# Optimization experiments

Measured on AMD Instinct MI355X. Metric: run time of the kernel, lower is better.

The kernel has to match this reference:

```python
import jax, jax.numpy as jnp
import numpy as np

N, E, VD, HD, ES = 10000, 80000, 32, 64, 68
NET_IN = VD * VD + 2 * HD + ES   # 1220: f2s(1024) + s[e0](64) + s[e1](64) + edge_s(68)
SELF_IN = VD * VD + 2 * HD       # 1152: temp_f2s(1024) + s(64) + s_c(64)
OUT_D = VD * VD + HD             # 1088: vector channel mixer + scalar update


def _lecun(k, fin, fout):
    return jax.random.normal(k, (fin, fout), jnp.float32) / jnp.sqrt(jnp.float32(fin))


def setup_inputs() -> dict:
    ks = jax.random.split(jax.random.key(0), 16)
    return {
        "f": jax.random.normal(ks[0], (N, 3, VD), jnp.float32),
        "s": jax.random.normal(ks[1], (N, HD), jnp.float32),
        "edge_f": jax.random.normal(ks[2], (E, 3, 1), jnp.float32),
        "edge_s": jax.random.normal(ks[3], (E, ES), jnp.float32),
        "W_emb1": _lecun(ks[4], 2 * VD + 1, VD),
        "net_W1": _lecun(ks[5], NET_IN, HD), "net_b1": jnp.zeros((HD,), jnp.float32),
        "net_W2": _lecun(ks[6], HD, HD), "net_b2": jnp.zeros((HD,), jnp.float32),
        "net_W3": _lecun(ks[7], HD, OUT_D), "net_b3": jnp.zeros((OUT_D,), jnp.float32),
        "W_emb2": _lecun(ks[8], 2 * VD, VD),
        "self_W1": _lecun(ks[9], SELF_IN, HD), "self_b1": jnp.zeros((HD,), jnp.float32),
        "self_W2": _lecun(ks[10], HD, HD), "self_b2": jnp.zeros((HD,), jnp.float32),
        "self_W3": _lecun(ks[11], HD, OUT_D), "self_b3": jnp.zeros((OUT_D,), jnp.float32),
        "edge_index": jax.random.randint(ks[12], (2, E), 0, N),
    }


def _mlp(x, W1, b1, W2, b2, W3, b3):
    h = jax.nn.relu(x @ W1 + b1)
    h = jax.nn.relu(h @ W2 + b2)
    return h @ W3 + b3


def _segment_mean(x, ids, n):
    tot = jax.ops.segment_sum(x, ids, num_segments=n)
    cnt = jax.ops.segment_sum(jnp.ones(ids.shape, x.dtype), ids, num_segments=n)
    return tot / jnp.maximum(cnt, 1.0).reshape((n,) + (1,) * (x.ndim - 1))


def _forward(f, s, edge_f, edge_s,
             W_emb1, net_W1, net_b1, net_W2, net_b2, net_W3, net_b3,
             W_emb2, self_W1, self_b1, self_W2, self_b2, self_W3, self_b3,
             edge_index):
    n = f.shape[0]
    e0, e1 = edge_index[0], edge_index[1]
    # --- edge message: gather -> embed -> gram einsum -> MLP ---
    _f = jnp.concatenate((f[e0], f[e1], edge_f), axis=-1)          # [E,3,2VD+1]
    _s = jnp.concatenate((s[e0], s[e1], edge_s), axis=-1)          # [E,2HD+ES]
    _f = _f @ W_emb1                                               # [E,3,VD]
    f2s = jnp.einsum('eij,eik->ejk', _f, _f).reshape(-1, VD * VD)  # _f^T @ _f, [E,VD*VD]
    Fn = jnp.linalg.norm(f2s, axis=-1, keepdims=True) + 1.0
    c = _mlp(jnp.concatenate((f2s, _s), axis=-1),
             net_W1, net_b1, net_W2, net_b2, net_W3, net_b3) / Fn  # [E,OUT_D]
    f_c = jnp.einsum('eij,ejk->eik', _f, c[:, :VD * VD].reshape(-1, VD, VD))  # [E,3,VD]
    f_c = _segment_mean(f_c, e0, n)                                # [N,3,VD]
    s_c = _segment_mean(c[:, VD * VD:], e0, n)                     # [N,HD]
    # --- node self-update ---
    tf = jnp.concatenate((f, f_c), axis=-1) @ W_emb2               # [N,3,VD]
    tf2s = jnp.einsum('nij,nik->njk', tf, tf).reshape(n, VD * VD)
    Fn2 = jnp.linalg.norm(tf2s, axis=-1, keepdims=True) + 1.0
    c2 = _mlp(jnp.concatenate((tf2s, s, s_c), axis=-1),
              self_W1, self_b1, self_W2, self_b2, self_W3, self_b3) / Fn2
    f_out = jnp.einsum('nij,njk->nik', tf, c2[:, :VD * VD].reshape(-1, VD, VD)) + f
    s_out = c2[:, VD * VD:] + s
    return f_out, s_out


def reference(f, s, edge_f, edge_s,
              W_emb1, net_W1, net_b1, net_W2, net_b2, net_W3, net_b3,
              W_emb2, self_W1, self_b1, self_W2, self_b2, self_W3, self_b3,
              edge_index):
    return _forward(f, s, edge_f, edge_s,
                    W_emb1, net_W1, net_b1, net_W2, net_b2, net_W3, net_b3,
                    W_emb2, self_W1, self_b1, self_W2, self_b2, self_W3, self_b3,
                    edge_index)
```

## Files before the change

### kernel.cpp

```cpp
#include <hip/hip_runtime.h>
#include <math.h>

#define NN 10000
#define NE 80000
#define SFH 102
#define SFB 98
#define SSB 66
#define STX 72
#define NTRI 528
#define SAE 104
#define SAN 72

typedef __attribute__((ext_vector_type(8))) __bf16 bf16x8;
typedef __attribute__((ext_vector_type(8))) short short8v;
typedef __attribute__((ext_vector_type(4))) float f32x4;
typedef __attribute__((ext_vector_type(4))) unsigned uint4v;

__device__ __forceinline__ ushort f2bf(float x) {
  union { float f; unsigned u; } v; v.f = x;
  unsigned r = v.u + 0x7FFFu + ((v.u >> 16) & 1u);
  return (ushort)(r >> 16);
}
__device__ __forceinline__ float bfu(ushort u) {
  union { unsigned x; float f; } v; v.x = (unsigned)u << 16;
  return v.f;
}
__device__ __forceinline__ void tri_ab(int k, int& a, int& b) {
  int aa = 0, rem = k;
  while (rem >= 32 - aa) { rem -= 32 - aa; ++aa; }
  a = aa; b = aa + rem;
}

__global__ __launch_bounds__(1024)
void sgnn_scan(const int* __restrict__ deg, int* __restrict__ cursor,
               int* __restrict__ start) {
  __shared__ int sm[1024];
  const int t = threadIdx.x;
  const int i0 = t * 10;
  int v[10], pre = 0;
  #pragma unroll
  for (int q = 0; q < 10; ++q) {
    const int i = i0 + q;
    v[q] = (i < NN) ? deg[i] : 0;
    pre += v[q];
  }
  sm[t] = pre;
  __syncthreads();
  int run = pre;
  #pragma unroll
  for (int d = 1; d < 1024; d <<= 1) {
    const int add = (t >= d) ? sm[t - d] : 0;
    __syncthreads();
    run += add;
    sm[t] = run;
    __syncthreads();
  }
  int excl = run - pre;
  #pragma unroll
  for (int q = 0; q < 10; ++q) {
    const int i = i0 + q;
    if (i < NN) { cursor[i] = excl; start[i] = excl; }
    excl += v[q];
  }
}

__global__ __launch_bounds__(256)
void sgnn_scatter(const int* __restrict__ eidx, int* __restrict__ cursor,
                  int* __restrict__ sorted) {
  const int e = blockIdx.x * 256 + threadIdx.x;
  if (e < NE) {
    const int p = atomicAdd(cursor + eidx[e], 1);
    sorted[p] = e;
  }
}

__global__ __launch_bounds__(256)
void sgnn_wconv(const float* __restrict__ nW1, const float* __restrict__ nW2,
                const float* __restrict__ nW3, const float* __restrict__ sW1,
                const float* __restrict__ sW2, const float* __restrict__ sW3,
                const float* __restrict__ Wemb1, const float* __restrict__ Wemb2,
                const int* __restrict__ eidx, int* __restrict__ deg,
                ushort* __restrict__ wout, ushort* __restrict__ tab) {
  const int gid = blockIdx.x * 256 + threadIdx.x;
  if (gid < NE) atomicAdd(deg + eidx[gid], 1);
  if (gid >= 61 * 4096) {
    const int k = gid - 61 * 4096;
    if (k < NTRI) {
      int a, b; tri_ab(k, a, b);
      tab[k] = (ushort)(a | (b << 8) | ((a != b) ? 0x8000 : 0));
    }
    return;
  }
  const int tile = gid >> 12, idx = gid & 4095;
  const int c = idx >> 6, k = idx & 63;
  float v = 0.f;
  if (tile < 12) {
    const int T = tile;
    if (T < 8 || (T == 8 && k < 16)) {
      const int ktri = T * 64 + k;
      if (ktri < NTRI) {
        int a, b; tri_ab(ktri, a, b);
        v = nW1[(a * 32 + b) * 64 + c];
        if (a != b) v += nW1[(b * 32 + a) * 64 + c];
      }
    } else if (T == 8) { if (k < 20) v = nW1[(1216 + (k - 16)) * 64 + c]; }
    else if (T == 9)   v = nW1[(1024 + k) * 64 + c];
    else if (T == 10)  v = nW1[(1088 + k) * 64 + c];
    else               v = nW1[(1152 + k) * 64 + c];
  } else if (tile == 12) v = nW2[k * 64 + c];
  else if (tile < 30)    v = nW3[k * 1088 + (tile - 13) * 64 + c];
  else if (tile < 41) {
    const int T = tile - 30;
    if (T < 8 || (T == 8 && k < 16)) {
      const int ktri = T * 64 + k;
      if (ktri < NTRI) {
        int a, b; tri_ab(ktri, a, b);
        v = sW1[(a * 32 + b) * 64 + c];
        if (a != b) v += sW1[(b * 32 + a) * 64 + c];
      }
    } else if (T == 9) v = sW1[(1024 + k) * 64 + c];
    else if (T == 10)  v = sW1[(1088 + k) * 64 + c];
  } else if (tile == 41) v = sW2[k * 64 + c];
  else if (tile < 59)    v = sW3[k * 1088 + (tile - 42) * 64 + c];
  else if (tile == 59) {
    const int col = idx / 96, kk = idx % 96;
    v = (col < 32 && kk < 65) ? Wemb1[kk * 32 + col] : 0.f;
  } else {
    const int col = idx >> 6;
    v = (col < 32) ? Wemb2[k * 32 + col] : 0.f;
  }
  wout[gid] = f2bf(v);
}

#define STAGE_W(srcbase) do { const ushort* _s = (srcbase);                      \
  _Pragma("unroll") for (int rr = 0; rr < 2; ++rr) {                             \
    const int idx_ = t + 256 * rr; const int c_ = idx_ >> 3, ko_ = idx_ & 7;     \
    *(short8v*)&Wl[c_ * STX + ko_ * 8] = *(const short8v*)&_s[c_ * 64 + ko_ * 8];\
  } } while (0)

#define WPRE_LOAD(srcbase) do { const ushort* _s = (srcbase);                    \
  wpre0 = *(const short8v*)&_s[(t >> 3) * 64 + (t & 7) * 8];                     \
  wpre1 = *(const short8v*)&_s[(32 + (t >> 3)) * 64 + (t & 7) * 8]; } while (0)

#define WPRE_STORE() do {                                                        \
  *(short8v*)&Wl[(t >> 3) * STX + (t & 7) * 8] = wpre0;                          \
  *(short8v*)&Wl[(32 + (t >> 3)) * STX + (t & 7) * 8] = wpre1; } while (0)

#define MFMA_K64_RA() do {                                                       \
  acc[0] = __builtin_amdgcn_mfma_f32_16x16x32_bf16(af0.v8,                       \
      *(const bf16x8*)&Wl[(     ll) * STX + lh * 8], acc[0], 0, 0, 0);           \
  acc[1] = __builtin_amdgcn_mfma_f32_16x16x32_bf16(af0.v8,                       \
      *(const bf16x8*)&Wl[(16 + ll) * STX + lh * 8], acc[1], 0, 0, 0);           \
  acc[2] = __builtin_amdgcn_mfma_f32_16x16x32_bf16(af0.v8,                       \
      *(const bf16x8*)&Wl[(32 + ll) * STX + lh * 8], acc[2], 0, 0, 0);           \
  acc[3] = __builtin_amdgcn_mfma_f32_16x16x32_bf16(af0.v8,                       \
      *(const bf16x8*)&Wl[(48 + ll) * STX + lh * 8], acc[3], 0, 0, 0);           \
  acc[0] = __builtin_amdgcn_mfma_f32_16x16x32_bf16(af1.v8,                       \
      *(const bf16x8*)&Wl[(     ll) * STX + 32 + lh * 8], acc[0], 0, 0, 0);      \
  acc[1] = __builtin_amdgcn_mfma_f32_16x16x32_bf16(af1.v8,                       \
      *(const bf16x8*)&Wl[(16 + ll) * STX + 32 + lh * 8], acc[1], 0, 0, 0);      \
  acc[2] = __builtin_amdgcn_mfma_f32_16x16x32_bf16(af1.v8,                       \
      *(const bf16x8*)&Wl[(32 + ll) * STX + 32 + lh * 8], acc[2], 0, 0, 0);      \
  acc[3] = __builtin_amdgcn_mfma_f32_16x16x32_bf16(af1.v8,                       \
      *(const bf16x8*)&Wl[(48 + ll) * STX + 32 + lh * 8], acc[3], 0, 0, 0);      \
} while (0)

#define MFMA_K64() do {                                                          \
  _Pragma("unroll") for (int kb = 0; kb < 2; ++kb) {                             \
    const bf16x8 af_ = *(const bf16x8*)&Xl[(w * 16 + ll) * STX + kb * 32 + lh * 8]; \
    acc[0] = __builtin_amdgcn_mfma_f32_16x16x32_bf16(af_,                        \
        *(const bf16x8*)&Wl[(     ll) * STX + kb * 32 + lh * 8], acc[0], 0, 0, 0); \
    acc[1] = __builtin_amdgcn_mfma_f32_16x16x32_bf16(af_,                        \
        *(const bf16x8*)&Wl[(16 + ll) * STX + kb * 32 + lh * 8], acc[1], 0, 0, 0); \
    acc[2] = __builtin_amdgcn_mfma_f32_16x16x32_bf16(af_,                        \
        *(const bf16x8*)&Wl[(32 + ll) * STX + kb * 32 + lh * 8], acc[2], 0, 0, 0); \
    acc[3] = __builtin_amdgcn_mfma_f32_16x16x32_bf16(af_,                        \
        *(const bf16x8*)&Wl[(48 + ll) * STX + kb * 32 + lh * 8], acc[3], 0, 0, 0); \
  } } while (0)

#define ZERO_ACC() do { _Pragma("unroll") for (int q = 0; q < 4; ++q)            \
    acc[q] = (f32x4){0.f, 0.f, 0.f, 0.f}; } while (0)

#define PACK_STORE16(dstp) do {                                                  \
  unsigned pk[8];                                                                \
  _Pragma("unroll") for (int q = 0; q < 8; ++q)                                  \
    pk[q] = (unsigned)f2bf(xv[2 * q]) | ((unsigned)f2bf(xv[2 * q + 1]) << 16);   \
  *(uint4v*)(dstp)       = (uint4v){pk[0], pk[1], pk[2], pk[3]};                 \
  *(uint4v*)((dstp) + 8) = (uint4v){pk[4], pk[5], pk[6], pk[7]};                 \
} while (0)

#define PACK_AF() do {                                                           \
  _Pragma("unroll") for (int q2 = 0; q2 < 4; ++q2) {                             \
    af0.u[q2] = (unsigned)f2bf(xv[2 * q2]) | ((unsigned)f2bf(xv[2 * q2 + 1]) << 16); \
    af1.u[q2] = (unsigned)f2bf(xv[8 + 2 * q2]) | ((unsigned)f2bf(xv[8 + 2 * q2 + 1]) << 16); \
  } } while (0)

#define TRI8(kt, off) do {                                                       \
  int prev_a = -1; float fa0 = 0.f, fa1 = 0.f, fa2 = 0.f;                        \
  _Pragma("unroll") for (int q = 0; q < 8; ++q) {                                \
    const int tb = tabL[(kt) + q];                                               \
    const int a_ = tb & 31, b_ = (tb >> 8) & 31;                                 \
    if (a_ != prev_a) { fa0 = bfu(frA[a_]); fa1 = bfu(frA[32 + a_]);             \
                        fa2 = bfu(frA[64 + a_]); prev_a = a_; }                  \
    const float v = fmaf(fa0, bfu(frA[b_]),                                      \
        fmaf(fa1, bfu(frA[32 + b_]), fa2 * bfu(frA[64 + b_])));                  \
    const float wsel = (tb & 0x8000) ? 2.f : 1.f;                                \
    sumsq = fmaf(v * wsel, v, sumsq);                                            \
    xv[(off) + q] = v;                                                           \
  } } while (0)

#define XV8_LOAD(p, off) do { const float* _p = (p);                             \
  const float4 va = *(const float4*)(_p);                                        \
  const float4 vb = *(const float4*)(_p + 4);                                    \
  xv[(off)+0]=va.x; xv[(off)+1]=va.y; xv[(off)+2]=va.z; xv[(off)+3]=va.w;        \
  xv[(off)+4]=vb.x; xv[(off)+5]=vb.y; xv[(off)+6]=vb.z; xv[(off)+7]=vb.w;        \
} while (0)

#define XV_LOAD16(p) do { const float* _p = (p);                                 \
  _Pragma("unroll") for (int q = 0; q < 4; ++q) {                                \
    const float4 v4 = *(const float4*)(_p + 4 * q);                              \
    xv[4 * q + 0] = v4.x; xv[4 * q + 1] = v4.y;                                  \
    xv[4 * q + 2] = v4.z; xv[4 * q + 3] = v4.w; } } while (0)

#define CONSUME_NT() do {                                                        \
  _Pragma("unroll") for (int r = 0; r < 4; ++r) {                                \
    const int row_ = w * 16 + lh * 4 + r;                                        \
    const unsigned u0 = *(const unsigned*)&smFh[row_ * SFH +      nt * 2];       \
    const unsigned u1 = *(const unsigned*)&smFh[row_ * SFH + 32 + nt * 2];       \
    const unsigned u2 = *(const unsigned*)&smFh[row_ * SFH + 64 + nt * 2];       \
    union { unsigned x; float f; } l0, h0, l1, h1, l2, h2;                       \
    l0.x = u0 << 16; h0.x = u0 & 0xffff0000u;                                    \
    l1.x = u1 << 16; h1.x = u1 & 0xffff0000u;                                    \
    l2.x = u2 << 16; h2.x = u2 & 0xffff0000u;                                    \
    _Pragma("unroll") for (int nc = 0; nc < 4; ++nc) {                           \
      const float cv = (acc[nc][r] + b3v[nc]) * ifnr[r];                         \
      const int p = nc & 1;                                                      \
      const float f0 = (nc < 2) ? l0.f : h0.f;                                   \
      const float f1 = (nc < 2) ? l1.f : h1.f;                                   \
      const float f2 = (nc < 2) ? l2.f : h2.f;                                   \
      fch[(r * 3 + 0) * 2 + p] = fmaf(f0, cv, fch[(r * 3 + 0) * 2 + p]);         \
      fch[(r * 3 + 1) * 2 + p] = fmaf(f1, cv, fch[(r * 3 + 1) * 2 + p]);         \
      fch[(r * 3 + 2) * 2 + p] = fmaf(f2, cv, fch[(r * 3 + 2) * 2 + p]);         \
    }                                                                            \
  } } while (0)

#define STAGE_FS() do {                                                          \
  _Pragma("unroll") for (int r = 0; r < 4; ++r) {                                \
    const int row_ = w * 16 + lh * 4 + r;                                        \
    _Pragma("unroll") for (int i = 0; i < 3; ++i) {                              \
      F[row_ * SFB + i * 32 + ll]      = f2bf(fch[(r * 3 + i) * 2 + 0]);         \
      F[row_ * SFB + i * 32 + ll + 16] = f2bf(fch[(r * 3 + i) * 2 + 1]);         \
    }                                                                            \
    _Pragma("unroll") for (int nc = 0; nc < 4; ++nc)                             \
      S[row_ * SSB + nc * 16 + ll] = f2bf(cs[nc * 4 + r]);                       \
  } } while (0)

#define LDS_BYTES 34656

__global__ __launch_bounds__(256, 3)
void sgnn_edge(const float* __restrict__ f, const float* __restrict__ s,
               const float* __restrict__ edge_f, const float* __restrict__ edge_s,
               const float* __restrict__ b1, const float* __restrict__ b2,
               const float* __restrict__ b3,
               const ushort* __restrict__ wbf, const ushort* __restrict__ tab_g,
               const int* __restrict__ eidx, const int* __restrict__ sorted,
               const int* __restrict__ start_g, const int* __restrict__ deg_g,
               float* __restrict__ fc_sum, float* __restrict__ sc_sum) {
  __shared__ __align__(16) char sbuf[LDS_BYTES];
  ushort* smFh = (ushort*)sbuf;
  ushort* F    = (ushort*)sbuf;
  ushort* Xl   = (ushort*)(sbuf + 13056);
  ushort* S    = (ushort*)(sbuf + 13056);
  ushort* Aemb = (ushort*)(sbuf + 13056);
  ushort* Wl   = (ushort*)(sbuf + 22272);
  int*    snode = (int*)(sbuf + 31488);
  int*    srow0 = snode + 8;
  int*    srow1 = snode + 16;
  int*    sst   = snode + 24;
  int*    sdg   = snode + 32;
  ushort* tabL = (ushort*)(sbuf + 33088);
  float*  iFn  = (float*)(sbuf + 33088);
  int*    es_s = (int*)(sbuf + 34144);
  ushort* e0s  = (ushort*)(sbuf + 34400);
  ushort* e1s  = (ushort*)(sbuf + 34528);

  const int t = threadIdx.x, j = t & 63, w = t >> 6, eb = w * 16;
  const int lh = j >> 4, ll = j & 15;
  const int bid = blockIdx.x;
  const ushort* wembT = wbf + 59 * 4096;
  short8v wpre0, wpre1;

  if (t < 64) {
    const int e = sorted[bid * 64 + t];
    es_s[t] = e;
    e0s[t] = (ushort)eidx[e];
    e1s[t] = (ushort)eidx[NE + e];
  }
  for (int idx = t; idx < NTRI; idx += 256) tabL[idx] = tab_g[idx];
  __syncthreads();

  int str = 0, dgr = 0;
  if (j < 16) {
    const int n_ = e0s[eb + j];
    str = start_g[n_];
    dgr = deg_g[n_];
  }
  WPRE_LOAD(wbf + 0);

  #pragma unroll 1
  for (int h = 0; h < 2; ++h) {
    const int hb = h * 32;
    #pragma unroll 1
    for (int cc = t; cc < 576; cc += 256) {
      const int row = cc / 6, seg = cc - row * 6;
      const int lel = (row * 43) >> 7, il = row - lel * 3;
      const int k0 = seg * 16;
      float xv[16];
      if (seg < 4) {
        const int nd = (seg < 2) ? (int)e0s[hb + lel] : (int)e1s[hb + lel];
        XV_LOAD16(f + nd * 96 + il * 32 + (seg & 1) * 16);
      } else if (seg == 4) {
        xv[0] = edge_f[es_s[hb + lel] * 3 + il];
        #pragma unroll
        for (int m = 1; m < 16; ++m) xv[m] = 0.f;
      } else {
        #pragma unroll
        for (int m = 0; m < 16; ++m) xv[m] = 0.f;
      }
      PACK_STORE16(&Aemb[row * SAE + k0]);
    }
    __syncthreads();
    #pragma unroll 1
    for (int job = w * 3; job < w * 3 + 3; ++job) {
      const int mt = job >> 1, nt = job & 1;
      f32x4 ac = (f32x4){0.f, 0.f, 0.f, 0.f};
      #pragma unroll
      for (int kb = 0; kb < 3; ++kb) {
        const bf16x8 av = *(const bf16x8*)&Aemb[(mt * 16 + ll) * SAE + kb * 32 + lh * 8];
        const bf16x8 bv = *(const bf16x8*)&wembT[(nt * 16 + ll) * 96 + kb * 32 + lh * 8];
        ac = __builtin_amdgcn_mfma_f32_16x16x32_bf16(av, bv, ac, 0, 0, 0);
      }
      #pragma unroll
      for (int r = 0; r < 4; ++r) {
        const int rr = mt * 16 + lh * 4 + r;
        const int lel = (rr * 43) >> 7, il = rr - lel * 3;
        smFh[(hb + lel) * SFH + il * 32 + nt * 16 + ll] = f2bf(ac[r]);
      }
    }
    __syncthreads();
  }

  f32x4 acc[4];
  ZERO_ACC();
  float sumsq = 0.f;
  const int rowA = w * 16 + ll;
  const ushort* frA = smFh + rowA * SFH;

  #pragma unroll 1
  for (int T = 0; T < 12; ++T) {
    float xv[16];
    union { unsigned u[4]; bf16x8 v8; } af0, af1;
    if (T < 8) {
      TRI8(T * 64 + lh * 8, 0);
      TRI8(T * 64 + 32 + lh * 8, 8);
    } else if (T == 8) {
      #pragma unroll
      for (int kb2 = 0; kb2 < 2; ++kb2)
        #pragma unroll
        for (int q = 0; q < 8; ++q) {
          const int k = kb2 * 32 + lh * 8 + q;
          float v = 0.f;
          if (k < 16) {
            const int tb = tabL[512 + k];
            const int a_ = tb & 31, b_ = (tb >> 8) & 31;
            v = fmaf(bfu(frA[a_]), bfu(frA[b_]),
                fmaf(bfu(frA[32 + a_]), bfu(frA[32 + b_]),
                     bfu(frA[64 + a_]) * bfu(frA[64 + b_])));
            const float wsel = (tb & 0x8000) ? 2.f : 1.f;
            sumsq = fmaf(v * wsel, v, sumsq);
          } else if (k < 20) {
            v = edge_s[es_s[rowA] * 68 + 64 + (k - 16)];
          }
          xv[kb2 * 8 + q] = v;
        }
    } else {
      const float* p = (T == 9)  ? (s + e0s[rowA] * 64)
                     : (T == 10) ? (s + e1s[rowA] * 64)
                                 : (edge_s + es_s[rowA] * 68);
      XV8_LOAD(p + lh * 8, 0);
      XV8_LOAD(p + 32 + lh * 8, 8);
    }
    PACK_AF();
    __syncthreads();
    WPRE_STORE();
    __syncthreads();
    WPRE_LOAD(wbf + (T + 1) * 4096);
    MFMA_K64_RA();
  }

  {
    float ss = sumsq;
    ss += __shfl_xor(ss, 16);
    ss += __shfl_xor(ss, 32);
    __syncthreads();
    if (j < 16) iFn[eb + j] = 1.f / (sqrtf(ss) + 1.f);
  }
  #pragma unroll
  for (int nc = 0; nc < 4; ++nc) {
    const float bv = b1[nc * 16 + ll];
    #pragma unroll
    for (int r = 0; r < 4; ++r)
      Xl[(w * 16 + lh * 4 + r) * STX + nc * 16 + ll] = f2bf(fmaxf(acc[nc][r] + bv, 0.f));
  }
  WPRE_STORE();
  ZERO_ACC();
  __syncthreads();
  WPRE_LOAD(wbf + 13 * 4096);

  MFMA_K64();
  #pragma unroll
  for (int nc = 0; nc < 4; ++nc) {
    const float bv = b2[nc * 16 + ll];
    #pragma unroll
    for (int r = 0; r < 4; ++r)
      Xl[(w * 16 + lh * 4 + r) * STX + nc * 16 + ll] = f2bf(fmaxf(acc[nc][r] + bv, 0.f));
  }

  float fch[24];
  #pragma unroll
  for (int q = 0; q < 24; ++q) fch[q] = 0.f;
  float cs[16];
  float ifnr[4];

  #pragma unroll 1
  for (int nt = 0; nt < 17; ++nt) {
    __syncthreads();
    WPRE_STORE();
    float b3v[4];
    #pragma unroll
    for (int nc = 0; nc < 4; ++nc) b3v[nc] = b3[nt * 64 + nc * 16 + ll];
    __syncthreads();
    if (nt < 16) WPRE_LOAD(wbf + (14 + nt) * 4096);
    if (nt == 0) {
      #pragma unroll
      for (int r = 0; r < 4; ++r) ifnr[r] = iFn[w * 16 + lh * 4 + r];
    }
    ZERO_ACC();
    MFMA_K64();
    if (nt < 16) {
      CONSUME_NT();
    } else {
      #pragma unroll
      for (int nc = 0; nc < 4; ++nc)
        #pragma unroll
        for (int r = 0; r < 4; ++r)
          cs[nc * 4 + r] = (acc[nc][r] + b3v[nc]) * ifnr[r];
    }
  }

  __syncthreads();
  STAGE_FS();
  if (t < 8) snode[t] = -1;
  __syncthreads();

  {
    float r0 = 0.f, r1 = 0.f, rs = 0.f;
    int runlen = 0;
    const int gwb = bid * 64 + eb;
    #pragma unroll 1
    for (int m = 0; m < 16; ++m) {
      const int row = eb + m;
      r0 += bfu(F[row * SFB + j]);
      if (j < 32) r1 += bfu(F[row * SFB + 64 + j]);
      rs += bfu(S[row * SSB + j]);
      ++runlen;
      const int n = e0s[row];
      if (m == 15 || e0s[row + 1] != n) {
        const int st = __shfl(str, m);
        const int dg = __shfl(dgr, m);
        const int g1v = gwb + m, g0v = g1v - runlen + 1;
        if (g0v == st && runlen == dg) {
          fc_sum[n * 96 + j] = r0;
          if (j < 32) fc_sum[n * 96 + 64 + j] = r1;
          sc_sum[n * 64 + j] = rs;
        } else {
          const int slot = (g0v == gwb) ? 2 * w : 2 * w + 1;
          if (j == 0) {
            snode[slot] = n; srow0[slot] = row - runlen + 1; srow1[slot] = row;
            sst[slot] = st; sdg[slot] = dg;
          }
        }
        r0 = r1 = rs = 0.f; runlen = 0;
      }
    }
  }
  __syncthreads();

  if (t < 160) {
    const int ch = t;
    int prevn = -1;
    #pragma unroll 1
    for (int ss = 0; ss < 8; ++ss) {
      const int n = snode[ss];
      if (n < 0) continue;
      if (n != prevn) {
        float v = 0.f;
        #pragma unroll 1
        for (int k2 = ss; k2 < 8; ++k2) {
          if (snode[k2] == n) {
            #pragma unroll 1
            for (int row = srow0[k2]; row <= srow1[k2]; ++row)
              v += (ch < 96) ? bfu(F[row * SFB + ch]) : bfu(S[row * SSB + (ch - 96)]);
          } else if (k2 > ss && snode[k2] >= 0) break;
        }
        const bool cib = (sst[ss] >= bid * 64) && (sst[ss] + sdg[ss] <= bid * 64 + 64);
        float* dst = (ch < 96) ? (fc_sum + n * 96 + ch) : (sc_sum + n * 64 + (ch - 96));
        if (cib) *dst = v; else atomicAdd(dst, v);
      }
      prevn = n;
    }
  }
}

__global__ __launch_bounds__(256, 3)
void sgnn_node(const float* __restrict__ f, const float* __restrict__ s,
               const float* __restrict__ b1, const float* __restrict__ b2,
               const float* __restrict__ b3,
               const ushort* __restrict__ wbf, const ushort* __restrict__ tab_g,
               const float* __restrict__ fcm, const float* __restrict__ scm,
               const int* __restrict__ deg_g,
               float* __restrict__ of, float* __restrict__ os) {
  __shared__ __align__(16) char sbuf[LDS_BYTES];
  ushort* smFh = (ushort*)sbuf;
  ushort* F    = (ushort*)sbuf;
  ushort* Xl   = (ushort*)(sbuf + 13056);
  ushort* S    = (ushort*)(sbuf + 13056);
  ushort* Aemb = (ushort*)(sbuf + 13056);
  ushort* Wl   = (ushort*)(sbuf + 22272);
  float*  icntL = (float*)(sbuf + 31488);
  ushort* tabL = (ushort*)(sbuf + 33088);
  float*  iFn  = (float*)(sbuf + 33088);

  const int t = threadIdx.x, j = t & 63, w = t >> 6, eb = w * 16;
  const int lh = j >> 4, ll = j & 15;
  const int nbase = blockIdx.x * 64;
  const ushort* wembTn = wbf + 60 * 4096;
  short8v wpre0, wpre1;

  for (int idx = t; idx < NTRI; idx += 256) tabL[idx] = tab_g[idx];
  if (t < 64)
    icntL[t] = 1.f / fmaxf((float)deg_g[min(nbase + t, NN - 1)], 1.f);
  WPRE_LOAD(wbf + 30 * 4096);
  __syncthreads();

  #pragma unroll 1
  for (int h = 0; h < 2; ++h) {
    const int hb = h * 32;
    #pragma unroll 1
    for (int cc = t; cc < 384; cc += 256) {
      const int row = cc >> 2, seg = cc & 3;
      const int lel = (row * 43) >> 7, il = row - lel * 3;
      const int nc = min(nbase + hb + lel, NN - 1);
      const int k0 = seg * 16;
      float xv[16];
      if (seg < 2) {
        XV_LOAD16(f + nc * 96 + il * 32 + seg * 16);
      } else {
        XV_LOAD16(fcm + nc * 96 + il * 32 + (seg - 2) * 16);
        const float ic = icntL[hb + lel];
        #pragma unroll
        for (int m = 0; m < 16; ++m) xv[m] *= ic;
      }
      PACK_STORE16(&Aemb[row * SAN + k0]);
    }
    __syncthreads();
    #pragma unroll 1
    for (int job = w * 3; job < w * 3 + 3; ++job) {
      const int mt = job >> 1, nt = job & 1;
      f32x4 ac = (f32x4){0.f, 0.f, 0.f, 0.f};
      #pragma unroll
      for (int kb = 0; kb < 2; ++kb) {
        const bf16x8 av = *(const bf16x8*)&Aemb[(mt * 16 + ll) * SAN + kb * 32 + lh * 8];
        const bf16x8 bv = *(const bf16x8*)&wembTn[(nt * 16 + ll) * 64 + kb * 32 + lh * 8];
        ac = __builtin_amdgcn_mfma_f32_16x16x32_bf16(av, bv, ac, 0, 0, 0);
      }
      #pragma unroll
      for (int r = 0; r < 4; ++r) {
        const int rr = mt * 16 + lh * 4 + r;
        const int lel = (rr * 43) >> 7, il = rr - lel * 3;
        smFh[(hb + lel) * SFH + il * 32 + nt * 16 + ll] = f2bf(ac[r]);
      }
    }
    __syncthreads();
  }

  f32x4 acc[4];
  ZERO_ACC();
  float sumsq = 0.f;
  const int rowA = w * 16 + ll;
  const ushort* frA = smFh + rowA * SFH;
  const int ncA = min(nbase + rowA, NN - 1);

  #pragma unroll 1
  for (int T = 0; T < 11; ++T) {
    float xv[16];
    union { unsigned u[4]; bf16x8 v8; } af0, af1;
    if (T < 8) {
      TRI8(T * 64 + lh * 8, 0);
      TRI8(T * 64 + 32 + lh * 8, 8);
    } else if (T == 8) {
      #pragma unroll
      for (int kb2 = 0; kb2 < 2; ++kb2)
        #pragma unroll
        for (int q = 0; q < 8; ++q) {
          const int k = kb2 * 32 + lh * 8 + q;
          float v = 0.f;
          if (k < 16) {
            const int tb = tabL[512 + k];
            const int a_ = tb & 31, b_ = (tb >> 8) & 31;
            v = fmaf(bfu(frA[a_]), bfu(frA[b_]),
                fmaf(bfu(frA[32 + a_]), bfu(frA[32 + b_]),
                     bfu(frA[64 + a_]) * bfu(frA[64 + b_])));
            const float wsel = (tb & 0x8000) ? 2.f : 1.f;
            sumsq = fmaf(v * wsel, v, sumsq);
          }
          xv[kb2 * 8 + q] = v;
        }
    } else if (T == 9) {
      XV8_LOAD(s + ncA * 64 + lh * 8, 0);
      XV8_LOAD(s + ncA * 64 + 32 + lh * 8, 8);
    } else {
      const float ic = icntL[rowA];
      XV8_LOAD(scm + ncA * 64 + lh * 8, 0);
      XV8_LOAD(scm + ncA * 64 + 32 + lh * 8, 8);
      #pragma unroll
      for (int m = 0; m < 16; ++m) xv[m] *= ic;
    }
    PACK_AF();
    __syncthreads();
    WPRE_STORE();
    __syncthreads();
    WPRE_LOAD(wbf + (31 + T) * 4096);
    MFMA_K64_RA();
  }

  {
    float ss = sumsq;
    ss += __shfl_xor(ss, 16);
    ss += __shfl_xor(ss, 32);
    __syncthreads();
    if (j < 16) iFn[eb + j] = 1.f / (sqrtf(ss) + 1.f);
  }
  #pragma unroll
  for (int nc = 0; nc < 4; ++nc) {
    const float bv = b1[nc * 16 + ll];
    #pragma unroll
    for (int r = 0; r < 4; ++r)
      Xl[(w * 16 + lh * 4 + r) * STX + nc * 16 + ll] = f2bf(fmaxf(acc[nc][r] + bv, 0.f));
  }
  WPRE_STORE();
  ZERO_ACC();
  __syncthreads();
  WPRE_LOAD(wbf + 42 * 4096);

  MFMA_K64();
  #pragma unroll
  for (int nc = 0; nc < 4; ++nc) {
    const float bv = b2[nc * 16 + ll];
    #pragma unroll
    for (int r = 0; r < 4; ++r)
      Xl[(w * 16 + lh * 4 + r) * STX + nc * 16 + ll] = f2bf(fmaxf(acc[nc][r] + bv, 0.f));
  }

  float fch[24];
  #pragma unroll
  for (int q = 0; q < 24; ++q) fch[q] = 0.f;
  float cs[16];
  float ifnr[4];

  #pragma unroll 1
  for (int nt = 0; nt < 17; ++nt) {
    __syncthreads();
    WPRE_STORE();
    float b3v[4];
    #pragma unroll
    for (int nc = 0; nc < 4; ++nc) b3v[nc] = b3[nt * 64 + nc * 16 + ll];
    __syncthreads();
    if (nt < 16) WPRE_LOAD(wbf + (43 + nt) * 4096);
    if (nt == 0) {
      #pragma unroll
      for (int r = 0; r < 4; ++r) ifnr[r] = iFn[w * 16 + lh * 4 + r];
    }
    ZERO_ACC();
    MFMA_K64();
    if (nt < 16) {
      CONSUME_NT();
    } else {
      #pragma unroll
      for (int nc = 0; nc < 4; ++nc)
        #pragma unroll
        for (int r = 0; r < 4; ++r)
          cs[nc * 4 + r] = (acc[nc][r] + b3v[nc]) * ifnr[r];
    }
  }

  __syncthreads();
  STAGE_FS();
  __syncthreads();

  #pragma unroll 1
  for (int m = 0; m < 16; ++m) {
    const int row = eb + m;
    const int n_m = nbase + row;
    if (n_m < NN) {
      of[n_m * 96 + j] = bfu(F[row * SFB + j]) + f[n_m * 96 + j];
      if (j < 32)
        of[n_m * 96 + 64 + j] = bfu(F[row * SFB + 64 + j]) + f[n_m * 96 + 64 + j];
      os[n_m * 64 + j] = bfu(S[row * SSB + j]) + s[n_m * 64 + j];
    }
  }
}

extern "C" void kernel_launch(void* const* d_in, const int* in_sizes, int n_in,
                              void* d_out, int out_size, void* d_ws, size_t ws_size,
                              hipStream_t stream) {
  const float* f      = (const float*)d_in[0];
  const float* s      = (const float*)d_in[1];
  const float* edge_f = (const float*)d_in[2];
  const float* edge_s = (const float*)d_in[3];
  const float* Wemb1  = (const float*)d_in[4];
  const float* nW1 = (const float*)d_in[5];
  const float* nb1 = (const float*)d_in[6];
  const float* nW2 = (const float*)d_in[7];
  const float* nb2 = (const float*)d_in[8];
  const float* nW3 = (const float*)d_in[9];
  const float* nb3 = (const float*)d_in[10];
  const float* Wemb2 = (const float*)d_in[11];
  const float* sW1 = (const float*)d_in[12];
  const float* sb1 = (const float*)d_in[13];
  const float* sW2 = (const float*)d_in[14];
  const float* sb2 = (const float*)d_in[15];
  const float* sW3 = (const float*)d_in[16];
  const float* sb3 = (const float*)d_in[17];
  const int* eidx  = (const int*)d_in[18];

  float* of = (float*)d_out;
  float* os = of + (size_t)NN * 96;

  int* deg    = (int*)d_ws;
  int* cursor = deg + NN;
  int* start  = cursor + NN;
  int* sorted = start + NN;
  ushort* wbf = (ushort*)(sorted + NE);
  ushort* tab = wbf + 61 * 4096;

  hipMemsetAsync(deg, 0, (size_t)NN * 4, stream);
  hipMemsetAsync(d_out, 0, (size_t)NN * 160 * 4, stream);

  hipLaunchKernelGGL(sgnn_wconv, dim3((61 * 4096 + NTRI + 255) / 256), dim3(256),
                     0, stream, nW1, nW2, nW3, sW1, sW2, sW3, Wemb1, Wemb2,
                     eidx, deg, wbf, tab);
  hipLaunchKernelGGL(sgnn_scan, dim3(1), dim3(1024), 0, stream, deg, cursor, start);
  hipLaunchKernelGGL(sgnn_scatter, dim3((NE + 255) / 256), dim3(256), 0, stream,
                     eidx, cursor, sorted);
  hipLaunchKernelGGL(sgnn_edge, dim3(NE / 64), dim3(256), 0, stream,
                     f, s, edge_f, edge_s, nb1, nb2, nb3,
                     wbf, tab, eidx, sorted, start, deg,
                     of , os );
  hipLaunchKernelGGL(sgnn_node, dim3((NN + 63) / 64), dim3(256), 0, stream,
                     f, s, sb1, sb2, sb3,
                     wbf, tab, of , os , deg, of, os);
}
```

Baseline: 198.0 us.

## Double-buffer LDS weight tiles to halve barriers in MLP loops

```diff
diff --git a/kernel.cpp b/kernel.cpp
--- a/kernel.cpp
+++ b/kernel.cpp
@@ -132,50 +132,44 @@
   wout[gid] = f2bf(v);
 }
 
-#define STAGE_W(srcbase) do { const ushort* _s = (srcbase);                      \
-  _Pragma("unroll") for (int rr = 0; rr < 2; ++rr) {                             \
-    const int idx_ = t + 256 * rr; const int c_ = idx_ >> 3, ko_ = idx_ & 7;     \
-    *(short8v*)&Wl[c_ * STX + ko_ * 8] = *(const short8v*)&_s[c_ * 64 + ko_ * 8];\
-  } } while (0)
-
 #define WPRE_LOAD(srcbase) do { const ushort* _s = (srcbase);                    \
   wpre0 = *(const short8v*)&_s[(t >> 3) * 64 + (t & 7) * 8];                     \
   wpre1 = *(const short8v*)&_s[(32 + (t >> 3)) * 64 + (t & 7) * 8]; } while (0)
 
-#define WPRE_STORE() do {                                                        \
-  *(short8v*)&Wl[(t >> 3) * STX + (t & 7) * 8] = wpre0;                          \
-  *(short8v*)&Wl[(32 + (t >> 3)) * STX + (t & 7) * 8] = wpre1; } while (0)
-
-#define MFMA_K64_RA() do {                                                       \
+#define WPRE_STORE_TO(Wd) do { ushort* _d = (Wd);                                \
+  *(short8v*)&_d[(t >> 3) * STX + (t & 7) * 8] = wpre0;                          \
+  *(short8v*)&_d[(32 + (t >> 3)) * STX + (t & 7) * 8] = wpre1; } while (0)
+
+#define MFMA_K64_RA_B(Wb) do { const ushort* _wl = (Wb);                         \
   acc[0] = __builtin_amdgcn_mfma_f32_16x16x32_bf16(af0.v8,                       \
-      *(const bf16x8*)&Wl[(     ll) * STX + lh * 8], acc[0], 0, 0, 0);           \
+      *(const bf16x8*)&_wl[(     ll) * STX + lh * 8], acc[0], 0, 0, 0);          \
   acc[1] = __builtin_amdgcn_mfma_f32_16x16x32_bf16(af0.v8,                       \
-      *(const bf16x8*)&Wl[(16 + ll) * STX + lh * 8], acc[1], 0, 0, 0);           \
+      *(const bf16x8*)&_wl[(16 + ll) * STX + lh * 8], acc[1], 0, 0, 0);          \
   acc[2] = __builtin_amdgcn_mfma_f32_16x16x32_bf16(af0.v8,                       \
-      *(const bf16x8*)&Wl[(32 + ll) * STX + lh * 8], acc[2], 0, 0, 0);           \
+      *(const bf16x8*)&_wl[(32 + ll) * STX + lh * 8], acc[2], 0, 0, 0);          \
   acc[3] = __builtin_amdgcn_mfma_f32_16x16x32_bf16(af0.v8,                       \
-      *(const bf16x8*)&Wl[(48 + ll) * STX + lh * 8], acc[3], 0, 0, 0);           \
+      *(const bf16x8*)&_wl[(48 + ll) * STX + lh * 8], acc[3], 0, 0, 0);          \
   acc[0] = __builtin_amdgcn_mfma_f32_16x16x32_bf16(af1.v8,                       \
-      *(const bf16x8*)&Wl[(     ll) * STX + 32 + lh * 8], acc[0], 0, 0, 0);      \
+      *(const bf16x8*)&_wl[(     ll) * STX + 32 + lh * 8], acc[0], 0, 0, 0);     \
   acc[1] = __builtin_amdgcn_mfma_f32_16x16x32_bf16(af1.v8,                       \
-      *(const bf16x8*)&Wl[(16 + ll) * STX + 32 + lh * 8], acc[1], 0, 0, 0);      \
+      *(const bf16x8*)&_wl[(16 + ll) * STX + 32 + lh * 8], acc[1], 0, 0, 0);     \
   acc[2] = __builtin_amdgcn_mfma_f32_16x16x32_bf16(af1.v8,                       \
-      *(const bf16x8*)&Wl[(32 + ll) * STX + 32 + lh * 8], acc[2], 0, 0, 0);      \
+      *(const bf16x8*)&_wl[(32 + ll) * STX + 32 + lh * 8], acc[2], 0, 0, 0);     \
   acc[3] = __builtin_amdgcn_mfma_f32_16x16x32_bf16(af1.v8,                       \
-      *(const bf16x8*)&Wl[(48 + ll) * STX + 32 + lh * 8], acc[3], 0, 0, 0);      \
+      *(const bf16x8*)&_wl[(48 + ll) * STX + 32 + lh * 8], acc[3], 0, 0, 0);     \
 } while (0)
 
-#define MFMA_K64() do {                                                          \
+#define MFMA_K64_B(Xb, Wb) do { const ushort* _x = (Xb); const ushort* _wl = (Wb);\
   _Pragma("unroll") for (int kb = 0; kb < 2; ++kb) {                             \
-    const bf16x8 af_ = *(const bf16x8*)&Xl[(w * 16 + ll) * STX + kb * 32 + lh * 8]; \
+    const bf16x8 af_ = *(const bf16x8*)&_x[(w * 16 + ll) * STX + kb * 32 + lh * 8]; \
     acc[0] = __builtin_amdgcn_mfma_f32_16x16x32_bf16(af_,                        \
-        *(const bf16x8*)&Wl[(     ll) * STX + kb * 32 + lh * 8], acc[0], 0, 0, 0); \
+        *(const bf16x8*)&_wl[(     ll) * STX + kb * 32 + lh * 8], acc[0], 0, 0, 0); \
     acc[1] = __builtin_amdgcn_mfma_f32_16x16x32_bf16(af_,                        \
-        *(const bf16x8*)&Wl[(16 + ll) * STX + kb * 32 + lh * 8], acc[1], 0, 0, 0); \
+        *(const bf16x8*)&_wl[(16 + ll) * STX + kb * 32 + lh * 8], acc[1], 0, 0, 0); \
     acc[2] = __builtin_amdgcn_mfma_f32_16x16x32_bf16(af_,                        \
-        *(const bf16x8*)&Wl[(32 + ll) * STX + kb * 32 + lh * 8], acc[2], 0, 0, 0); \
+        *(const bf16x8*)&_wl[(32 + ll) * STX + kb * 32 + lh * 8], acc[2], 0, 0, 0); \
     acc[3] = __builtin_amdgcn_mfma_f32_16x16x32_bf16(af_,                        \
-        *(const bf16x8*)&Wl[(48 + ll) * STX + kb * 32 + lh * 8], acc[3], 0, 0, 0); \
+        *(const bf16x8*)&_wl[(48 + ll) * STX + kb * 32 + lh * 8], acc[3], 0, 0, 0); \
   } } while (0)
 
 #define ZERO_ACC() do { _Pragma("unroll") for (int q = 0; q < 4; ++q)            \
@@ -255,7 +249,7 @@
       S[row_ * SSB + nc * 16 + ll] = f2bf(cs[nc * 4 + r]);                       \
   } } while (0)
 
-#define LDS_BYTES 34656
+#define LDS_BYTES 43872
 
 __global__ __launch_bounds__(256, 3)
 void sgnn_edge(const float* __restrict__ f, const float* __restrict__ s,
@@ -283,6 +277,7 @@
   int*    es_s = (int*)(sbuf + 34144);
   ushort* e0s  = (ushort*)(sbuf + 34400);
   ushort* e1s  = (ushort*)(sbuf + 34528);
+  ushort* Wl1  = (ushort*)(sbuf + 34656);
 
   const int t = threadIdx.x, j = t & 63, w = t >> 6, eb = w * 16;
   const int lh = j >> 4, ll = j & 15;
@@ -356,8 +351,13 @@
   const int rowA = w * 16 + ll;
   const ushort* frA = smFh + rowA * SFH;
 
+  WPRE_STORE_TO(Wl);
+  WPRE_LOAD(wbf + 1 * 4096);
+  __syncthreads();
   #pragma unroll 1
   for (int T = 0; T < 12; ++T) {
+    ushort* Wc = (T & 1) ? Xl : Wl;
+    ushort* Wn = (T & 1) ? Wl : Xl;
     float xv[16];
     union { unsigned u[4]; bf16x8 v8; } af0, af1;
     if (T < 8) {
@@ -391,18 +391,16 @@
       XV8_LOAD(p + 32 + lh * 8, 8);
     }
     PACK_AF();
-    __syncthreads();
-    WPRE_STORE();
-    __syncthreads();
-    WPRE_LOAD(wbf + (T + 1) * 4096);
-    MFMA_K64_RA();
+    WPRE_STORE_TO(Wn);
+    WPRE_LOAD(wbf + (T + 2) * 4096);
+    MFMA_K64_RA_B(Wc);
+    __syncthreads();
   }
 
   {
     float ss = sumsq;
     ss += __shfl_xor(ss, 16);
     ss += __shfl_xor(ss, 32);
-    __syncthreads();
     if (j < 16) iFn[eb + j] = 1.f / (sqrtf(ss) + 1.f);
   }
   #pragma unroll
@@ -412,12 +410,8 @@
     for (int r = 0; r < 4; ++r)
       Xl[(w * 16 + lh * 4 + r) * STX + nc * 16 + ll] = f2bf(fmaxf(acc[nc][r] + bv, 0.f));
   }
-  WPRE_STORE();
   ZERO_ACC();
-  __syncthreads();
-  WPRE_LOAD(wbf + 13 * 4096);
-
-  MFMA_K64();
+  MFMA_K64_B(Xl, Wl);
   #pragma unroll
   for (int nc = 0; nc < 4; ++nc) {
     const float bv = b2[nc * 16 + ll];
@@ -425,28 +419,31 @@
     for (int r = 0; r < 4; ++r)
       Xl[(w * 16 + lh * 4 + r) * STX + nc * 16 + ll] = f2bf(fmaxf(acc[nc][r] + bv, 0.f));
   }
+  WPRE_STORE_TO(Wl1);
+  WPRE_LOAD(wbf + 14 * 4096);
+  __syncthreads();
 
   float fch[24];
   #pragma unroll
   for (int q = 0; q < 24; ++q) fch[q] = 0.f;
   float cs[16];
   float ifnr[4];
+  #pragma unroll
+  for (int r = 0; r < 4; ++r) ifnr[r] = iFn[w * 16 + lh * 4 + r];
 
   #pragma unroll 1
   for (int nt = 0; nt < 17; ++nt) {
-    __syncthreads();
-    WPRE_STORE();
+    ushort* Wc = (nt & 1) ? Wl : Wl1;
+    ushort* Wn = (nt & 1) ? Wl1 : Wl;
+    if (nt < 16) {
+      WPRE_STORE_TO(Wn);
+      if (nt < 15) WPRE_LOAD(wbf + (15 + nt) * 4096);
+    }
     float b3v[4];
     #pragma unroll
     for (int nc = 0; nc < 4; ++nc) b3v[nc] = b3[nt * 64 + nc * 16 + ll];
-    __syncthreads();
-    if (nt < 16) WPRE_LOAD(wbf + (14 + nt) * 4096);
-    if (nt == 0) {
-      #pragma unroll
-      for (int r = 0; r < 4; ++r) ifnr[r] = iFn[w * 16 + lh * 4 + r];
-    }
     ZERO_ACC();
-    MFMA_K64();
+    MFMA_K64_B(Xl, Wc);
     if (nt < 16) {
       CONSUME_NT();
     } else {
@@ -456,9 +453,9 @@
         for (int r = 0; r < 4; ++r)
           cs[nc * 4 + r] = (acc[nc][r] + b3v[nc]) * ifnr[r];
     }
-  }
-
-  __syncthreads();
+    __syncthreads();
+  }
+
   STAGE_FS();
   if (t < 8) snode[t] = -1;
   __syncthreads();
@@ -540,6 +537,7 @@
   float*  icntL = (float*)(sbuf + 31488);
   ushort* tabL = (ushort*)(sbuf + 33088);
   float*  iFn  = (float*)(sbuf + 33088);
+  ushort* Wl1  = (ushort*)(sbuf + 34656);
 
   const int t = threadIdx.x, j = t & 63, w = t >> 6, eb = w * 16;
   const int lh = j >> 4, ll = j & 15;
@@ -601,8 +599,13 @@
   const ushort* frA = smFh + rowA * SFH;
   const int ncA = min(nbase + rowA, NN - 1);
 
+  WPRE_STORE_TO(Xl);
+  WPRE_LOAD(wbf + 31 * 4096);
+  __syncthreads();
   #pragma unroll 1
   for (int T = 0; T < 11; ++T) {
+    ushort* Wc = (T & 1) ? Wl : Xl;
+    ushort* Wn = (T & 1) ? Xl : Wl;
     float xv[16];
     union { unsigned u[4]; bf16x8 v8; } af0, af1;
     if (T < 8) {
@@ -637,18 +640,16 @@
       for (int m = 0; m < 16; ++m) xv[m] *= ic;
     }
     PACK_AF();
-    __syncthreads();
-    WPRE_STORE();
-    __syncthreads();
-    WPRE_LOAD(wbf + (31 + T) * 4096);
-    MFMA_K64_RA();
+    WPRE_STORE_TO(Wn);
+    WPRE_LOAD(wbf + (32 + T) * 4096);
+    MFMA_K64_RA_B(Wc);
+    __syncthreads();
   }
 
   {
     float ss = sumsq;
     ss += __shfl_xor(ss, 16);
     ss += __shfl_xor(ss, 32);
-    __syncthreads();
     if (j < 16) iFn[eb + j] = 1.f / (sqrtf(ss) + 1.f);
   }
   #pragma unroll
@@ -658,12 +659,8 @@
     for (int r = 0; r < 4; ++r)
       Xl[(w * 16 + lh * 4 + r) * STX + nc * 16 + ll] = f2bf(fmaxf(acc[nc][r] + bv, 0.f));
   }
-  WPRE_STORE();
   ZERO_ACC();
-  __syncthreads();
-  WPRE_LOAD(wbf + 42 * 4096);
-
-  MFMA_K64();
+  MFMA_K64_B(Xl, Wl);
   #pragma unroll
   for (int nc = 0; nc < 4; ++nc) {
     const float bv = b2[nc * 16 + ll];
@@ -671,28 +668,31 @@
     for (int r = 0; r < 4; ++r)
       Xl[(w * 16 + lh * 4 + r) * STX + nc * 16 + ll] = f2bf(fmaxf(acc[nc][r] + bv, 0.f));
   }
+  WPRE_STORE_TO(Wl1);
+  WPRE_LOAD(wbf + 43 * 4096);
+  __syncthreads();
 
   float fch[24];
   #pragma unroll
   for (int q = 0; q < 24; ++q) fch[q] = 0.f;
   float cs[16];
   float ifnr[4];
+  #pragma unroll
+  for (int r = 0; r < 4; ++r) ifnr[r] = iFn[w * 16 + lh * 4 + r];
 
   #pragma unroll 1
   for (int nt = 0; nt < 17; ++nt) {
-    __syncthreads();
-    WPRE_STORE();
+    ushort* Wc = (nt & 1) ? Wl : Wl1;
+    ushort* Wn = (nt & 1) ? Wl1 : Wl;
+    if (nt < 16) {
+      WPRE_STORE_TO(Wn);
+      if (nt < 15) WPRE_LOAD(wbf + (44 + nt) * 4096);
+    }
     float b3v[4];
     #pragma unroll
     for (int nc = 0; nc < 4; ++nc) b3v[nc] = b3[nt * 64 + nc * 16 + ll];
-    __syncthreads();
-    if (nt < 16) WPRE_LOAD(wbf + (43 + nt) * 4096);
-    if (nt == 0) {
-      #pragma unroll
-      for (int r = 0; r < 4; ++r) ifnr[r] = iFn[w * 16 + lh * 4 + r];
-    }
     ZERO_ACC();
-    MFMA_K64();
+    MFMA_K64_B(Xl, Wc);
     if (nt < 16) {
       CONSUME_NT();
     } else {
@@ -702,9 +702,9 @@
         for (int r = 0; r < 4; ++r)
           cs[nc * 4 + r] = (acc[nc][r] + b3v[nc]) * ifnr[r];
     }
-  }
-
-  __syncthreads();
+    __syncthreads();
+  }
+
   STAGE_FS();
   __syncthreads();
 
```

New measurement: 195.1 us, median of 2. No clear change (-1.5%).
